# Kernel optimization log

Measured on AMD Instinct MI355X. Metric: run time of the kernel, lower is better.

Reference implementation:

```python
import jax, jax.numpy as jnp
import numpy as np

IOU_THRESH = 0.5


def _conv(x, w, b):
    y = jax.lax.conv_general_dilated(
        x, w, window_strides=(1, 1), padding='SAME',
        dimension_numbers=('NCHW', 'OIHW', 'NCHW'))
    return jax.nn.relu(y + b[None, :, None, None])


def _nms_keep(boxes):
    # boxes: [N,4] xyxy, sorted by descending score. Returns bool keep mask [N].
    x1, y1, x2, y2 = boxes[:, 0], boxes[:, 1], boxes[:, 2], boxes[:, 3]
    area = jnp.maximum(x2 - x1, 0.0) * jnp.maximum(y2 - y1, 0.0)
    xx1 = jnp.maximum(x1[:, None], x1[None, :])
    yy1 = jnp.maximum(y1[:, None], y1[None, :])
    xx2 = jnp.minimum(x2[:, None], x2[None, :])
    yy2 = jnp.minimum(y2[:, None], y2[None, :])
    inter = jnp.maximum(xx2 - xx1, 0.0) * jnp.maximum(yy2 - yy1, 0.0)
    iou = inter / (area[:, None] + area[None, :] - inter + 1e-9)  # [N,N]
    n = boxes.shape[0]
    idx = jnp.arange(n)

    def body(i, keep):
        # suppress later boxes that overlap box i too much, if i itself is kept
        suppress = (iou[i] > IOU_THRESH) & (idx > i) & keep[i]
        return keep & ~suppress

    return jax.lax.fori_loop(0, n, body, jnp.ones((n,), dtype=bool))


def setup_inputs() -> dict:
    key = jax.random.key(0)
    k = jax.random.split(key, 7)
    B, N = 32, 100
    x = jax.random.normal(k[0], (B, 3, 224, 224), dtype=jnp.float32)
    boxes = jax.random.uniform(k[1], (B, N, 4), dtype=jnp.float32) * 224.0
    scores = jax.random.uniform(k[2], (B, N), dtype=jnp.float32)
    w1 = jax.random.normal(k[3], (64, 3, 3, 3), dtype=jnp.float32) * (1.0 / np.sqrt(3 * 9))
    b1 = jnp.zeros((64,), dtype=jnp.float32)
    w2 = jax.random.normal(k[4], (128, 64, 3, 3), dtype=jnp.float32) * (1.0 / np.sqrt(64 * 9))
    b2 = jnp.zeros((128,), dtype=jnp.float32)
    return {'x': x, 'boxes': boxes, 'scores': scores,
            'w1': w1, 'b1': b1, 'w2': w2, 'b2': b2}


def reference(x, boxes, scores, w1, b1, w2, b2):
    # backbone: conv-relu-conv-relu-globalavgpool-flatten -> [B,128]
    h = _conv(x, w1, b1)
    h = _conv(h, w2, b2)
    feats = jnp.mean(h, axis=(2, 3))  # AdaptiveAvgPool2d((1,1)) + Flatten

    # per-image sort by descending score
    order = jnp.argsort(-scores, axis=1)                         # [B,N]
    boxes_sorted = jnp.take_along_axis(boxes, order[..., None], axis=1)
    scores_sorted = jnp.take_along_axis(scores, order, axis=1)

    # batched greedy NMS; fixed-shape keep mask instead of ragged index lists
    keep = jax.vmap(_nms_keep)(boxes_sorted)                     # [B,N] bool

    final_boxes = jnp.where(keep[..., None], boxes_sorted, 0.0)
    final_scores = jnp.where(keep, scores_sorted, 0.0)
    return feats, final_boxes, final_scores, keep
```

## Files before the change

### kernel.cpp

```cpp
#include <hip/hip_runtime.h>
#include <hip/hip_bf16.h>

#define HH 224
#define WW 224

#define OUT_FEATS  0
#define OUT_BOXES  4096
#define OUT_SCORES 16896
#define OUT_KEEP   20096

typedef __attribute__((ext_vector_type(8))) short short8;
typedef __attribute__((ext_vector_type(4))) float f32x4;
typedef __attribute__((ext_vector_type(16))) float f32x16;
typedef __attribute__((ext_vector_type(4))) unsigned int u32x4;
typedef __attribute__((ext_vector_type(2))) unsigned int u32x2;

static __device__ __forceinline__ unsigned short f2bf(float f) {
    __hip_bfloat16 h = __float2bfloat16(f);
    return *(unsigned short*)&h;
}

static __device__ __forceinline__ void gload_lds16(const void* g, void* l) {
    __builtin_amdgcn_global_load_lds(
        (const __attribute__((address_space(1))) unsigned int*)g,
        (__attribute__((address_space(3))) unsigned int*)l, 16, 0, 0);
}

__global__ void w2_convert(const float* __restrict__ w2, unsigned short* __restrict__ w2t)
{
    int t = blockIdx.x * 256 + threadIdx.x;
    if (t >= 9 * 128 * 64) return;
    int e     = t & 7;
    int oc    = (t >> 3) & 127;
    int kslot = (t >> 10) & 7;
    int tap   = t >> 13;
    int ic    = kslot * 8 + e;
    w2t[t] = f2bf(w2[(oc * 64 + ic) * 9 + tap]);
}

__global__ void w1_convert(const float* __restrict__ w1, unsigned short* __restrict__ w1bf)
{
    int t = blockIdx.x * 256 + threadIdx.x;
    if (t >= 64 * 32) return;
    int oc = t >> 5, k = t & 31;
    unsigned short v = 0;
    if (k < 27) v = f2bf(w1[oc * 27 + k]);
    w1bf[t] = v;
}

__global__ __launch_bounds__(256) void fused_conv_kernel(const float* __restrict__ x,
                                                         const unsigned short* __restrict__ w1bf,
                                                         const float* __restrict__ b1,
                                                         const unsigned short* __restrict__ w2t,
                                                         const float* __restrict__ b2,
                                                         float* __restrict__ partial)
{
    const int xt = blockIdx.x, yt = blockIdx.y, b = blockIdx.z;
    const int x0 = xt * 16, ty0 = yt * 16;
    const int tid = threadIdx.x;
    const int w = tid >> 6, lane = tid & 63;
    const int wp = w >> 1, wn = w & 1;
    const int l15 = lane & 15, lq = lane >> 4;
    const int l31 = lane & 31, hi = lane >> 5;

    __shared__ char smem[74240];
    char*  halo  = smem;
    char*  wlds0 = smem + 41472;
    char*  wlds1 = smem + 41472 + 16384;
    float* xpatch = (float*)wlds1;

#pragma unroll
    for (int it = 0; it < 4; ++it) {
        int c = it * 256 + tid;
        gload_lds16((const char*)w2t + c * 16, wlds0 + c * 16);
    }

    for (int i = tid; i < 1568; i += 256) {
        float v = 0.f;
        if (i < 1200) {
            int ic = i / 400; int rem = i - ic * 400;
            int r = rem / 20, c = rem - r * 20;
            int gy = ty0 - 2 + r, gx = x0 - 2 + c;
            if (gy >= 0 && gy < HH && gx >= 0 && gx < WW)
                v = x[((b * 3 + ic) * HH + gy) * WW + gx];
        }
        xpatch[i] = v;
    }

    short8 aw[4];
#pragma unroll
    for (int f = 0; f < 4; f++)
        aw[f] = *(const short8*)(w1bf + (f * 16 + l15) * 32 + lq * 8);
    float bias1[4][4];
#pragma unroll
    for (int f = 0; f < 4; f++)
#pragma unroll
        for (int j = 0; j < 4; j++)
            bias1[f][j] = b1[f * 16 + lq * 4 + j];

    int koff[8];
#pragma unroll
    for (int j = 0; j < 8; j++) {
        int k = lq * 8 + j;
        int ic = (k >= 18) ? 2 : (k >= 9 ? 1 : 0);
        int t = k - ic * 9;
        int dy = (t >= 6) ? 2 : (t >= 3 ? 1 : 0);
        int dx = t - dy * 3;
        koff[j] = (k < 27) ? ((ic * 20 + dy) * 20 + dx) * 4 : 4800;
    }
    __syncthreads();

    const char* xpb = (const char*)xpatch;
    for (int g = w; g < 21; g += 4) {
        int px0 = g * 16 + l15;
        int px = px0 > 323 ? 323 : px0;
        int row = (px * 456) >> 13;
        int col = px - row * 18;
        int rofs = row * 80 + col * 4;

        float pv[8];
#pragma unroll
        for (int j = 0; j < 8; j++)
            pv[j] = *(const float*)(xpb + (koff[j] + rofs));
        short8 bp;
        unsigned int* bpu = (unsigned int*)&bp;
#pragma unroll
        for (int jj = 0; jj < 4; jj++)
            bpu[jj] = (unsigned int)f2bf(pv[2 * jj]) | ((unsigned int)f2bf(pv[2 * jj + 1]) << 16);

        int gy = ty0 + row - 1, gx = x0 + col - 1;
        float vm = (gy >= 0 && gy < HH && gx >= 0 && gx < WW) ? 1.f : 0.f;
        bool wr = (px0 < 324);

#pragma unroll
        for (int f = 0; f < 4; f++) {
            f32x4 c = __builtin_amdgcn_mfma_f32_16x16x32_bf16(aw[f], bp,
                        (f32x4){0.f, 0.f, 0.f, 0.f}, 0, 0, 0);
            float v0 = fmaxf(c[0] + bias1[f][0], 0.f) * vm;
            float v1 = fmaxf(c[1] + bias1[f][1], 0.f) * vm;
            float v2 = fmaxf(c[2] + bias1[f][2], 0.f) * vm;
            float v3 = fmaxf(c[3] + bias1[f][3], 0.f) * vm;
            if (wr) {
                u32x2 pk;
                pk.x = (unsigned int)f2bf(v0) | ((unsigned int)f2bf(v1) << 16);
                pk.y = (unsigned int)f2bf(v2) | ((unsigned int)f2bf(v3) << 16);
                int byte = (f * 2 + (lq >> 1)) * 5184 + px * 16 + (lq & 1) * 8;
                *(u32x2*)(halo + byte) = pk;
            }
        }
    }
    __syncthreads();

    f32x16 acc[4][2];
#pragma unroll
    for (int mf = 0; mf < 4; mf++)
#pragma unroll
        for (int nf = 0; nf < 2; nf++)
#pragma unroll
            for (int q = 0; q < 16; q++)
                acc[mf][nf][q] = 0.f;

#pragma unroll
    for (int t = 0; t < 9; ++t) {
        if (t < 8) {
            char* wdst = ((t + 1) & 1) ? wlds1 : wlds0;
            const char* wsrc = (const char*)w2t + (t + 1) * 16384;
#pragma unroll
            for (int it = 0; it < 4; ++it) {
                int c = it * 256 + tid;
                gload_lds16(wsrc + c * 16, wdst + c * 16);
            }
        }
        const int dy = t / 3, dx = t % 3;
        const char* wbuf = (t & 1) ? wlds1 : wlds0;

#pragma unroll
        for (int s16 = 0; s16 < 4; s16++) {
            const int kslot = s16 * 2 + hi;
            short8 bfr[2];
#pragma unroll
            for (int nf = 0; nf < 2; nf++) {
                int oc = wn * 64 + nf * 32 + l31;
                bfr[nf] = *(const short8*)(wbuf + kslot * 2048 + oc * 16);
            }
            short8 a[4];
#pragma unroll
            for (int mf = 0; mf < 4; mf++) {
                int pos = (wp * 8 + mf * 2 + (l31 >> 4) + dy) * 18 + (l31 & 15) + dx;
                a[mf] = *(const short8*)(halo + kslot * 5184 + pos * 16);
            }
#pragma unroll
            for (int mf = 0; mf < 4; mf++)
#pragma unroll
                for (int nf = 0; nf < 2; nf++)
                    acc[mf][nf] = __builtin_amdgcn_mfma_f32_32x32x16_bf16(a[mf], bfr[nf], acc[mf][nf], 0, 0, 0);
        }
        __syncthreads();
    }

    float s[2];
#pragma unroll
    for (int nf = 0; nf < 2; nf++) {
        float bias = b2[wn * 64 + nf * 32 + l31];
        float v = 0.f;
#pragma unroll
        for (int mf = 0; mf < 4; mf++)
#pragma unroll
            for (int q = 0; q < 16; q++)
                v += fmaxf(acc[mf][nf][q] + bias, 0.f);
        v += __shfl_xor(v, 32, 64);
        s[nf] = v;
    }

    float* red = (float*)halo;
    if (hi == 0) {
#pragma unroll
        for (int nf = 0; nf < 2; nf++)
            red[((wp * 2 + wn) * 2 + nf) * 32 + l31] = s[nf];
    }
    __syncthreads();
    if (tid < 128) {
        int oc = tid;
        int wn2 = oc >> 6, nf2 = (oc >> 5) & 1, c32 = oc & 31;
        float tot = red[((0 * 2 + wn2) * 2 + nf2) * 32 + c32] +
                    red[((1 * 2 + wn2) * 2 + nf2) * 32 + c32];
        int tile = yt * 14 + xt;
        partial[((size_t)b * 128 + oc) * 196 + tile] = tot;
    }
}

__global__ void feats_reduce(const float* __restrict__ partial, float* __restrict__ out)
{
    int t = blockIdx.x;
    int lane = threadIdx.x;
    float s = 0.f;
    for (int k = lane; k < 196; k += 64) s += partial[(size_t)t * 196 + k];
#pragma unroll
    for (int m = 32; m >= 1; m >>= 1) s += __shfl_xor(s, m, 64);
    if (lane == 0) out[t] = s * (1.f / 50176.f);
}

__global__ __launch_bounds__(128) void nms_kernel(const float* __restrict__ boxes,
                                                  const float* __restrict__ scores,
                                                  float* __restrict__ out)
{
    const int b = blockIdx.x;
    const int tid = threadIdx.x;
    __shared__ float rs[100];
    __shared__ float bx1[100], by1[100], bx2[100], by2[100];
    __shared__ float ss[100], sx1[100], sy1[100], sx2[100], sy2[100], sarea[100];
    __shared__ int keep_s[100];

    if (tid < 100) {
        rs[tid] = scores[b * 100 + tid];
        bx1[tid] = boxes[(b * 100 + tid) * 4 + 0];
        by1[tid] = boxes[(b * 100 + tid) * 4 + 1];
        bx2[tid] = boxes[(b * 100 + tid) * 4 + 2];
        by2[tid] = boxes[(b * 100 + tid) * 4 + 3];
    }
    __syncthreads();
    if (tid < 100) {
        float s = rs[tid];
        int r = 0;
        for (int j = 0; j < 100; j++) {
            float sj = rs[j];
            r += (sj > s) || (sj == s && j < tid);
        }
        ss[r] = s; sx1[r] = bx1[tid]; sy1[r] = by1[tid];
        sx2[r] = bx2[tid]; sy2[r] = by2[tid];
        keep_s[tid] = 1;
    }
    __syncthreads();
    if (tid < 100)
        sarea[tid] = fmaxf(sx2[tid] - sx1[tid], 0.f) * fmaxf(sy2[tid] - sy1[tid], 0.f);
    __syncthreads();

    for (int i = 0; i < 99; i++) {
        if (keep_s[i] && tid > i && tid < 100) {
            float xx1 = fmaxf(sx1[i], sx1[tid]);
            float yy1 = fmaxf(sy1[i], sy1[tid]);
            float xx2 = fminf(sx2[i], sx2[tid]);
            float yy2 = fminf(sy2[i], sy2[tid]);
            float inter = fmaxf(xx2 - xx1, 0.f) * fmaxf(yy2 - yy1, 0.f);
            float iou = inter / (sarea[i] + sarea[tid] - inter + 1e-9f);
            if (iou > 0.5f) keep_s[tid] = 0;
        }
        __syncthreads();
    }

    if (tid < 100) {
        int k = keep_s[tid];
        int gi = b * 100 + tid;
        out[OUT_BOXES + gi * 4 + 0] = k ? sx1[tid] : 0.f;
        out[OUT_BOXES + gi * 4 + 1] = k ? sy1[tid] : 0.f;
        out[OUT_BOXES + gi * 4 + 2] = k ? sx2[tid] : 0.f;
        out[OUT_BOXES + gi * 4 + 3] = k ? sy2[tid] : 0.f;
        out[OUT_SCORES + gi] = k ? ss[tid] : 0.f;
        out[OUT_KEEP + gi] = k ? 1.f : 0.f;
    }
}

extern "C" void kernel_launch(void* const* d_in, const int* in_sizes, int n_in,
                              void* d_out, int out_size, void* d_ws, size_t ws_size,
                              hipStream_t stream)
{
    const float* x      = (const float*)d_in[0];
    const float* boxes  = (const float*)d_in[1];
    const float* scores = (const float*)d_in[2];
    const float* w1     = (const float*)d_in[3];
    const float* b1     = (const float*)d_in[4];
    const float* w2     = (const float*)d_in[5];
    const float* b2     = (const float*)d_in[6];
    float* out = (float*)d_out;

    char* wsb = (char*)d_ws;
    unsigned short* w2t  = (unsigned short*)wsb;
    unsigned short* w1bf = (unsigned short*)(wsb + 9 * 128 * 64 * 2);
    float*          partial = (float*)(wsb + 9 * 128 * 64 * 2 + 64 * 32 * 2);

    w2_convert<<<(9 * 128 * 64 + 255) / 256, 256, 0, stream>>>(w2, w2t);
    w1_convert<<<8, 256, 0, stream>>>(w1, w1bf);

    fused_conv_kernel<<<dim3(14, 14, 32), 256, 0, stream>>>(x, w1bf, b1, w2t, b2, partial);

    feats_reduce<<<4096, 64, 0, stream>>>(partial, out + OUT_FEATS);
    nms_kernel<<<32, 128, 0, stream>>>(boxes, scores, out);
}
```

Baseline: 265.2 us.

## Split batch across two conv kernel variants with different tile shapes

Adds a second fused conv kernel that uses 16x8 tiles, 128 threads and less LDS, with a single weight buffer reloaded per tap. It processes the first 16 images, while the original 16x16-tile kernel handles the remaining 16. Both write into separate partial buffers that a modified reduction combines. This appears intended to compare or balance occupancy against halo overhead. The two kernels run back to back on one stream, so they do not overlap, and the smaller tile recomputes more conv1 halo.

```diff
diff --git a/kernel.cpp b/kernel.cpp
--- a/kernel.cpp
+++ b/kernel.cpp
@@ -48,14 +48,178 @@
     w1bf[t] = v;
 }
 
-__global__ __launch_bounds__(256) void fused_conv_kernel(const float* __restrict__ x,
-                                                         const unsigned short* __restrict__ w1bf,
-                                                         const float* __restrict__ b1,
-                                                         const unsigned short* __restrict__ w2t,
-                                                         const float* __restrict__ b2,
-                                                         float* __restrict__ partial)
+__global__ __launch_bounds__(128) void fused_conv_v14(const float* __restrict__ x,
+                                                      const unsigned short* __restrict__ w1bf,
+                                                      const float* __restrict__ b1,
+                                                      const unsigned short* __restrict__ w2t,
+                                                      const float* __restrict__ b2,
+                                                      float* __restrict__ partialA)
 {
     const int xt = blockIdx.x, yt = blockIdx.y, b = blockIdx.z;
+    const int x0 = xt * 16, ty0 = yt * 8;
+    const int tid = threadIdx.x;
+    const int w = tid >> 6, lane = tid & 63;
+    const int l15 = lane & 15, lq = lane >> 4;
+    const int l31 = lane & 31, hi = lane >> 5;
+
+    __shared__ char smem[39424];
+    char*  halo = smem;
+    char*  wlds = smem + 23040;
+    float* xpatch = (float*)wlds;
+
+    for (int i = tid; i < 928; i += 128) {
+        float v = 0.f;
+        if (i < 720) {
+            int ic = i / 240; int rem = i - ic * 240;
+            int r = rem / 20, c = rem - r * 20;
+            int gy = ty0 - 2 + r, gx = x0 - 2 + c;
+            if (gy >= 0 && gy < HH && gx >= 0 && gx < WW)
+                v = x[((b * 3 + ic) * HH + gy) * WW + gx];
+        }
+        xpatch[i] = v;
+    }
+
+    short8 aw[4];
+#pragma unroll
+    for (int f = 0; f < 4; f++)
+        aw[f] = *(const short8*)(w1bf + (f * 16 + l15) * 32 + lq * 8);
+    float bias1[4][4];
+#pragma unroll
+    for (int f = 0; f < 4; f++)
+#pragma unroll
+        for (int j = 0; j < 4; j++)
+            bias1[f][j] = b1[f * 16 + lq * 4 + j];
+
+    int koff[8];
+#pragma unroll
+    for (int j = 0; j < 8; j++) {
+        int k = lq * 8 + j;
+        int ic = (k >= 18) ? 2 : (k >= 9 ? 1 : 0);
+        int t = k - ic * 9;
+        int dy = (t >= 6) ? 2 : (t >= 3 ? 1 : 0);
+        int dx = t - dy * 3;
+        koff[j] = (k < 27) ? ((ic * 12 + dy) * 20 + dx) * 4 : 2880;
+    }
+    __syncthreads();
+
+    const char* xpb = (const char*)xpatch;
+    for (int g = w; g < 12; g += 2) {
+        int px0 = g * 16 + l15;
+        int px = px0 > 179 ? 179 : px0;
+        int row = (px * 456) >> 13;
+        int col = px - row * 18;
+        int rofs = row * 80 + col * 4;
+
+        float pv[8];
+#pragma unroll
+        for (int j = 0; j < 8; j++)
+            pv[j] = *(const float*)(xpb + (koff[j] + rofs));
+        short8 bp;
+        unsigned int* bpu = (unsigned int*)&bp;
+#pragma unroll
+        for (int jj = 0; jj < 4; jj++)
+            bpu[jj] = (unsigned int)f2bf(pv[2 * jj]) | ((unsigned int)f2bf(pv[2 * jj + 1]) << 16);
+
+        int gy = ty0 + row - 1, gx = x0 + col - 1;
+        float vm = (gy >= 0 && gy < HH && gx >= 0 && gx < WW) ? 1.f : 0.f;
+        bool wr = (px0 < 180);
+
+#pragma unroll
+        for (int f = 0; f < 4; f++) {
+            f32x4 c = __builtin_amdgcn_mfma_f32_16x16x32_bf16(aw[f], bp,
+                        (f32x4){0.f, 0.f, 0.f, 0.f}, 0, 0, 0);
+            float v0 = fmaxf(c[0] + bias1[f][0], 0.f) * vm;
+            float v1 = fmaxf(c[1] + bias1[f][1], 0.f) * vm;
+            float v2 = fmaxf(c[2] + bias1[f][2], 0.f) * vm;
+            float v3 = fmaxf(c[3] + bias1[f][3], 0.f) * vm;
+            if (wr) {
+                u32x2 pk;
+                pk.x = (unsigned int)f2bf(v0) | ((unsigned int)f2bf(v1) << 16);
+                pk.y = (unsigned int)f2bf(v2) | ((unsigned int)f2bf(v3) << 16);
+                int byte = (f * 2 + (lq >> 1)) * 2880 + px * 16 + (lq & 1) * 8;
+                *(u32x2*)(halo + byte) = pk;
+            }
+        }
+    }
+    __syncthreads();
+
+#pragma unroll
+    for (int it = 0; it < 8; ++it) {
+        int c = it * 128 + tid;
+        gload_lds16((const char*)w2t + c * 16, wlds + c * 16);
+    }
+    __syncthreads();
+
+    f32x16 acc[4][2];
+#pragma unroll
+    for (int mf = 0; mf < 4; mf++)
+#pragma unroll
+        for (int nf = 0; nf < 2; nf++)
+#pragma unroll
+            for (int q = 0; q < 16; q++)
+                acc[mf][nf][q] = 0.f;
+
+#pragma unroll
+    for (int t = 0; t < 9; ++t) {
+        const int dy = t / 3, dx = t % 3;
+#pragma unroll
+        for (int s16 = 0; s16 < 4; s16++) {
+            const int kslot = s16 * 2 + hi;
+            short8 bfr[2];
+#pragma unroll
+            for (int nf = 0; nf < 2; nf++) {
+                int oc = w * 64 + nf * 32 + l31;
+                bfr[nf] = *(const short8*)(wlds + kslot * 2048 + oc * 16);
+            }
+            short8 a[4];
+#pragma unroll
+            for (int mf = 0; mf < 4; mf++) {
+                int pos = (mf * 2 + (l31 >> 4) + dy) * 18 + (l31 & 15) + dx;
+                a[mf] = *(const short8*)(halo + kslot * 2880 + pos * 16);
+            }
+#pragma unroll
+            for (int mf = 0; mf < 4; mf++)
+#pragma unroll
+                for (int nf = 0; nf < 2; nf++)
+                    acc[mf][nf] = __builtin_amdgcn_mfma_f32_32x32x16_bf16(a[mf], bfr[nf], acc[mf][nf], 0, 0, 0);
+        }
+        __syncthreads();
+        if (t < 8) {
+            const char* wsrc = (const char*)w2t + (t + 1) * 16384;
+#pragma unroll
+            for (int it = 0; it < 8; ++it) {
+                int c = it * 128 + tid;
+                gload_lds16(wsrc + c * 16, wlds + c * 16);
+            }
+            __syncthreads();
+        }
+    }
+
+    const int tile = yt * 14 + xt;
+#pragma unroll
+    for (int nf = 0; nf < 2; nf++) {
+        float bias = b2[w * 64 + nf * 32 + l31];
+        float v = 0.f;
+#pragma unroll
+        for (int mf = 0; mf < 4; mf++)
+#pragma unroll
+            for (int q = 0; q < 16; q++)
+                v += fmaxf(acc[mf][nf][q] + bias, 0.f);
+        v += __shfl_xor(v, 32, 64);
+        if (hi == 0)
+            partialA[((size_t)b * 128 + w * 64 + nf * 32 + l31) * 392 + tile] = v;
+    }
+}
+
+__global__ __launch_bounds__(256) void fused_conv_v12(const float* __restrict__ x,
+                                                      const unsigned short* __restrict__ w1bf,
+                                                      const float* __restrict__ b1,
+                                                      const unsigned short* __restrict__ w2t,
+                                                      const float* __restrict__ b2,
+                                                      float* __restrict__ partialB)
+{
+    const int xt = blockIdx.x, yt = blockIdx.y, bl = blockIdx.z;
+    const int b = bl + 16;
     const int x0 = xt * 16, ty0 = yt * 16;
     const int tid = threadIdx.x;
     const int w = tid >> 6, lane = tid & 63;
@@ -225,16 +389,22 @@
         float tot = red[((0 * 2 + wn2) * 2 + nf2) * 32 + c32] +
                     red[((1 * 2 + wn2) * 2 + nf2) * 32 + c32];
         int tile = yt * 14 + xt;
-        partial[((size_t)b * 128 + oc) * 196 + tile] = tot;
-    }
-}
-
-__global__ void feats_reduce(const float* __restrict__ partial, float* __restrict__ out)
+        partialB[((size_t)bl * 128 + oc) * 196 + tile] = tot;
+    }
+}
+
+__global__ void feats_reduce(const float* __restrict__ pA, const float* __restrict__ pB,
+                             float* __restrict__ out)
 {
     int t = blockIdx.x;
     int lane = threadIdx.x;
     float s = 0.f;
-    for (int k = lane; k < 196; k += 64) s += partial[(size_t)t * 196 + k];
+    if (t < 2048) {
+        for (int k = lane; k < 392; k += 64) s += pA[(size_t)t * 392 + k];
+    } else {
+        int t2 = t - 2048;
+        for (int k = lane; k < 196; k += 64) s += pB[(size_t)t2 * 196 + k];
+    }
 #pragma unroll
     for (int m = 32; m >= 1; m >>= 1) s += __shfl_xor(s, m, 64);
     if (lane == 0) out[t] = s * (1.f / 50176.f);
@@ -315,14 +485,16 @@
 
     char* wsb = (char*)d_ws;
     unsigned short* w2t  = (unsigned short*)wsb;
-    unsigned short* w1bf = (unsigned short*)(wsb + 9 * 128 * 64 * 2);
-    float*          partial = (float*)(wsb + 9 * 128 * 64 * 2 + 64 * 32 * 2);
+    unsigned short* w1bf = (unsigned short*)(wsb + 147456);
+    float* partialA = (float*)(wsb + 147456 + 4096);
+    float* partialB = (float*)(wsb + 147456 + 4096 + 3211264);
 
     w2_convert<<<(9 * 128 * 64 + 255) / 256, 256, 0, stream>>>(w2, w2t);
     w1_convert<<<8, 256, 0, stream>>>(w1, w1bf);
 
-    fused_conv_kernel<<<dim3(14, 14, 32), 256, 0, stream>>>(x, w1bf, b1, w2t, b2, partial);
-
-    feats_reduce<<<4096, 64, 0, stream>>>(partial, out + OUT_FEATS);
+    fused_conv_v14<<<dim3(14, 28, 16), 128, 0, stream>>>(x, w1bf, b1, w2t, b2, partialA);
+    fused_conv_v12<<<dim3(14, 14, 16), 256, 0, stream>>>(x, w1bf, b1, w2t, b2, partialB);
+
+    feats_reduce<<<4096, 64, 0, stream>>>(partialA, partialB, out + OUT_FEATS);
     nms_kernel<<<32, 128, 0, stream>>>(boxes, scores, out);
 }
```

Result: slower. 288.2 us (+8.7%).
